# Optimization experiments

Hardware: AMD Instinct MI355X
Metric: run time of the kernel (lower is better)

## Reference

```python
import jax, jax.numpy as jnp
import numpy as np

N_NODES = 50000
N_EDGES = 800000
D = 256


def _mean_aggregate(x, src, tgt, num_nodes):
    # scatter-mean of source features onto target nodes: [N, D]
    summed = jax.ops.segment_sum(x[src], tgt, num_segments=num_nodes)
    count = jax.ops.segment_sum(jnp.ones((src.shape[0],), x.dtype), tgt,
                                num_segments=num_nodes)
    return summed / jnp.maximum(count, 1.0)[:, None]


def _sage_conv(x, src, tgt, W_l, b, W_r):
    # PyG SAGEConv (aggr='mean'): lin_l(mean_j x_j) + lin_r(x_i)
    agg = _mean_aggregate(x, src, tgt, x.shape[0])
    return agg @ W_l + b + x @ W_r


def setup_inputs() -> dict:
    key = jax.random.key(0)
    ks = jax.random.split(key, 8)
    s = 1.0 / np.sqrt(D)
    x = jax.random.normal(ks[0], (N_NODES, D), dtype=jnp.float32)
    edge_index = jax.random.randint(ks[1], (2, N_EDGES), 0, N_NODES, dtype=jnp.int64)
    return {
        "x": x,
        "edge_index": edge_index,
        "W1_l": jax.random.normal(ks[2], (D, D), dtype=jnp.float32) * s,
        "b1": jnp.zeros((D,), dtype=jnp.float32),
        "W1_r": jax.random.normal(ks[3], (D, D), dtype=jnp.float32) * s,
        "W2_l": jax.random.normal(ks[4], (D, D), dtype=jnp.float32) * s,
        "b2": jnp.zeros((D,), dtype=jnp.float32),
        "W2_r": jax.random.normal(ks[5], (D, D), dtype=jnp.float32) * s,
    }


def reference(x, edge_index, W1_l, b1, W1_r, W2_l, b2, W2_r):
    src, tgt = edge_index[0], edge_index[1]
    h = jax.nn.relu(_sage_conv(x, src, tgt, W1_l, b1, W1_r))
    return _sage_conv(h, src, tgt, W2_l, b2, W2_r)
```

## Files before the change

### kernel.cpp

```cpp
#include <hip/hip_runtime.h>
#include <hip/hip_bf16.h>

#define NN 50000
#define NE 800000
#define DD 256
#define KK 512
#define PAD 64
#define CSTR 16

#define FB 3125
#define CB 12500
#define WB 1024

typedef unsigned short u16;
typedef unsigned int   u32;
typedef unsigned char  u8;
typedef __attribute__((ext_vector_type(8))) __bf16 bf16x8;
typedef __attribute__((ext_vector_type(4))) float  f32x4;
typedef __attribute__((ext_vector_type(2))) float  f32x2;
typedef __attribute__((ext_vector_type(8))) u16    u16x8;
typedef __attribute__((ext_vector_type(4))) u16    u16x4;

#define GLOAD_LDS16(g, l) \
  __builtin_amdgcn_global_load_lds((const __attribute__((address_space(1))) void*)(g), \
                                   (__attribute__((address_space(3))) void*)(l), 16, 0, 0)

static __device__ __forceinline__ u16 f2bf(float f) {
  u32 u = __float_as_uint(f);
  u32 r = (u + 0x7FFFu + ((u >> 16) & 1u)) >> 16;
  return (u16)r;
}

__global__ void k_prep(const int* __restrict__ src, const int* __restrict__ tgt,
                       int* __restrict__ cnt, int* __restrict__ col,
                       const float* __restrict__ x, u16* __restrict__ x_bf,
                       u32* __restrict__ x_f8,
                       const float* __restrict__ W1l, const float* __restrict__ W1r,
                       const float* __restrict__ W2l, const float* __restrict__ W2r,
                       u16* __restrict__ Wc1T, u16* __restrict__ Wc2T) {
  const int b = blockIdx.x;
  if (b < FB) {
    int i = b * 256 + threadIdx.x;
    int t = tgt[i];
    int p = atomicAdd(&cnt[t * CSTR], 1);
    if (p < PAD) col[t * PAD + p] = src[i];
  } else if (b < FB + CB) {
    int i = (b - FB) * 256 + threadIdx.x;
    const float4 v = *reinterpret_cast<const float4*>(x + i * 4);
    u16x4 o; o.x = f2bf(v.x); o.y = f2bf(v.y); o.z = f2bf(v.z); o.w = f2bf(v.w);
    *reinterpret_cast<u16x4*>(x_bf + i * 4) = o;
    int pk = __builtin_amdgcn_cvt_pk_fp8_f32(v.x, v.y, 0, false);
    pk = __builtin_amdgcn_cvt_pk_fp8_f32(v.z, v.w, pk, true);
    x_f8[i] = (u32)pk;
  } else {
    int gid = (b - FB - CB) * 256 + threadIdx.x;
    int layer = gid >> 17;
    int idx = gid & 131071;
    int n = idx >> 9, k = idx & 511;
    const float* Wl = layer ? W2l : W1l;
    const float* Wr = layer ? W2r : W1r;
    u16* WcT = layer ? Wc2T : Wc1T;
    float v = (k < DD) ? Wl[k * DD + n] : Wr[(k - DD) * DD + n];
    int reg = k >> 6, ko = k & 63;
    int k2 = (reg << 6) + ((((ko >> 3) ^ (n & 7)) << 3)) + (ko & 7);
    WcT[n * KK + k2] = f2bf(v);
  }
}

__global__ void k_aggregate(const u8* __restrict__ feat8, const int* __restrict__ cnt,
                            const int* __restrict__ col, u16* __restrict__ out) {
  const int wave = threadIdx.x >> 6;
  const int lane = threadIdx.x & 63;
  const int half = lane >> 5;
  const int l32 = lane & 31;
  const int node = blockIdx.x * 4 + wave;
  int deg = cnt[node * CSTR];
  if (deg > PAD) deg = PAD;
  const int s = node * PAD, e = s + deg;
  const int fo = l32 * 8;
  float a[8] = {0.f, 0.f, 0.f, 0.f, 0.f, 0.f, 0.f, 0.f};

#define ACC8(vv)                                                       \
  {                                                                    \
    f32x2 p0 = __builtin_amdgcn_cvt_pk_f32_fp8((int)(vv).x, false);    \
    f32x2 p1 = __builtin_amdgcn_cvt_pk_f32_fp8((int)(vv).x, true);     \
    f32x2 p2 = __builtin_amdgcn_cvt_pk_f32_fp8((int)(vv).y, false);    \
    f32x2 p3 = __builtin_amdgcn_cvt_pk_f32_fp8((int)(vv).y, true);     \
    a[0] += p0.x; a[1] += p0.y; a[2] += p1.x; a[3] += p1.y;            \
    a[4] += p2.x; a[5] += p2.y; a[6] += p3.x; a[7] += p3.y;            \
  }

  int i = s + half;
  for (; i + 6 < e; i += 8) {
    int c0 = col[i], c1 = col[i + 2], c2 = col[i + 4], c3 = col[i + 6];
    uint2 v0 = *reinterpret_cast<const uint2*>(feat8 + c0 * DD + fo);
    uint2 v1 = *reinterpret_cast<const uint2*>(feat8 + c1 * DD + fo);
    uint2 v2 = *reinterpret_cast<const uint2*>(feat8 + c2 * DD + fo);
    uint2 v3 = *reinterpret_cast<const uint2*>(feat8 + c3 * DD + fo);
    ACC8(v0) ACC8(v1) ACC8(v2) ACC8(v3)
  }
  for (; i < e; i += 2) {
    uint2 v = *reinterpret_cast<const uint2*>(feat8 + col[i] * DD + fo);
    ACC8(v)
  }
#undef ACC8
#pragma unroll
  for (int j = 0; j < 8; ++j) a[j] += __shfl_xor(a[j], 32, 64);

  if (half == 0) {
    const float scale = (deg > 0) ? 1.0f / (float)deg : 0.0f;
    u16x8 o;
#pragma unroll
    for (int j = 0; j < 8; ++j) o[j] = f2bf(a[j] * scale);
    *reinterpret_cast<u16x8*>(out + node * DD + fo) = o;
  }
}

#define BM 64
#define BN 256
#define BK 64

template <int LAYER>
__global__ void k_gemm_fused(const u16* __restrict__ A0, const u16* __restrict__ A1,
                             const u16* __restrict__ WcT, const float* __restrict__ bias,
                             u16* __restrict__ outb, u8* __restrict__ outf8,
                             float* __restrict__ outf, int M) {
  __shared__ alignas(16) u16 lA[BM * BK];
  __shared__ alignas(16) u16 lB[BN * BK];
  const int tid = threadIdx.x;
  const int rowBase = blockIdx.x * BM;
  const int wave = tid >> 6, lane = tid & 63;
  const int wc = wave;
  const int l8 = lane >> 3;
  const int ch = lane & 7;

  f32x4 acc[4][4] = {};

  for (int k0 = 0; k0 < KK; k0 += BK) {
    if (k0) __syncthreads();
    const u16* Asrc = (k0 < DD) ? A0 : A1;
    const int kk = k0 & (DD - 1);
#pragma unroll
    for (int j = 0; j < 2; ++j) {
      int row = wave * 16 + j * 8 + l8;
      const u16* g = Asrc + (size_t)(rowBase + row) * DD + kk + ((ch ^ (row & 7)) << 3);
      GLOAD_LDS16(g, &lA[(wave * 16 + j * 8) * BK]);
    }
#pragma unroll
    for (int j = 0; j < 8; ++j) {
      int row = wave * 64 + j * 8 + l8;
      const u16* g = WcT + (size_t)row * KK + k0 + (ch << 3);
      GLOAD_LDS16(g, &lB[(wave * 64 + j * 8) * BK]);
    }
    __syncthreads();

#pragma unroll
    for (int ks = 0; ks < 2; ++ks) {
      const int kbyte = ks * 64 + (lane >> 4) * 16;
      bf16x8 af[4], bfg[4];
#pragma unroll
      for (int m = 0; m < 4; ++m) {
        int row = m * 16 + (lane & 15);
        af[m] = *reinterpret_cast<const bf16x8*>((const char*)lA + row * 128 + (kbyte ^ ((row & 7) << 4)));
      }
#pragma unroll
      for (int n = 0; n < 4; ++n) {
        int row = wc * 64 + n * 16 + (lane & 15);
        bfg[n] = *reinterpret_cast<const bf16x8*>((const char*)lB + row * 128 + (kbyte ^ ((row & 7) << 4)));
      }
#pragma unroll
      for (int m = 0; m < 4; ++m)
#pragma unroll
        for (int n = 0; n < 4; ++n)
          acc[m][n] = __builtin_amdgcn_mfma_f32_16x16x32_bf16(af[m], bfg[n], acc[m][n], 0, 0, 0);
    }
  }

  const int lrow = (lane >> 4) * 4;
  const int lcol = lane & 15;
#pragma unroll
  for (int n = 0; n < 4; ++n) {
    const int gcol = wc * 64 + n * 16 + lcol;
    const float bv = bias[gcol];
#pragma unroll
    for (int m = 0; m < 4; ++m) {
#pragma unroll
      for (int r = 0; r < 4; ++r) {
        const int grow = rowBase + m * 16 + lrow + r;
        if (grow < M) {
          float v = acc[m][n][r] + bv;
          if (LAYER == 1) {
            v = fmaxf(v, 0.0f);
            outb[grow * DD + gcol] = f2bf(v);
            int pk = __builtin_amdgcn_cvt_pk_fp8_f32(v, 0.0f, 0, false);
            outf8[grow * DD + gcol] = (u8)(pk & 0xff);
          } else {
            outf[grow * DD + gcol] = v;
          }
        }
      }
    }
  }
}

extern "C" void kernel_launch(void* const* d_in, const int* in_sizes, int n_in,
                              void* d_out, int out_size, void* d_ws, size_t ws_size,
                              hipStream_t stream) {
  const float* x    = (const float*)d_in[0];
  const int*   ei   = (const int*)d_in[1];
  const float* W1l  = (const float*)d_in[2];
  const float* b1   = (const float*)d_in[3];
  const float* W1r  = (const float*)d_in[4];
  const float* W2l  = (const float*)d_in[5];
  const float* b2   = (const float*)d_in[6];
  const float* W2r  = (const float*)d_in[7];
  float* out = (float*)d_out;

  const int* srcIdx = ei;
  const int* tgtIdx = ei + NE;

  char* ws = (char*)d_ws;
  int* cnt    = (int*)(ws + 0);
  int* col    = (int*)(ws + 3200000);
  u16* x_bf   = (u16*)(ws + 16000000);
  u16* h_bf   = (u16*)(ws + 41600000);
  u16* agg_bf = (u16*)(ws + 67200000);
  u8*  x_f8   = (u8*) (ws + 92800000);
  u8*  h_f8   = (u8*) (ws + 105600000);
  u16* Wc1T   = (u16*)(ws + 118400000);
  u16* Wc2T   = (u16*)(ws + 118662144);

  hipMemsetAsync(cnt, 0, NN * CSTR * sizeof(int), stream);
  k_prep<<<FB + CB + WB, 256, 0, stream>>>(srcIdx, tgtIdx, cnt, col, x, x_bf,
                                           (u32*)x_f8,
                                           W1l, W1r, W2l, W2r, Wc1T, Wc2T);

  const int ggrid = (NN + BM - 1) / BM;

  k_aggregate<<<NN / 4, 256, 0, stream>>>(x_f8, cnt, col, agg_bf);
  k_gemm_fused<1><<<ggrid, 256, 0, stream>>>(agg_bf, x_bf, Wc1T, b1, h_bf, h_f8, nullptr, NN);
  k_aggregate<<<NN / 4, 256, 0, stream>>>(h_f8, cnt, col, agg_bf);
  k_gemm_fused<2><<<ggrid, 256, 0, stream>>>(agg_bf, h_bf, Wc2T, b2, nullptr, nullptr, out, NN);
}
```

Baseline: 200.5 us.

## Double GEMM row tile and interleave edge-bucketing with feature conversion blocks

The fused GEMM row tile grows from 64 to 128 rows, so each B-weight tile loaded into LDS is reused across twice as many rows. A-fragments are now loaded per m-step rather than all held at once, and out-of-range rows are clamped for loads. Separately, the prep kernel interleaves the atomic edge-bucketing blocks with the x conversion blocks, so atomic-heavy and bandwidth-heavy work run at the same time. The cost is double the accumulator registers, which may lower occupancy, and half as many GEMM blocks.

```diff
diff --git a/kernel.cpp b/kernel.cpp
--- a/kernel.cpp
+++ b/kernel.cpp
@@ -11,6 +11,7 @@
 #define FB 3125
 #define CB 12500
 #define WB 1024
+#define PREP_GRID (2 * FB + (CB - FB) + WB)
 
 typedef unsigned short u16;
 typedef unsigned int   u32;
@@ -39,13 +40,25 @@
                        const float* __restrict__ W2l, const float* __restrict__ W2r,
                        u16* __restrict__ Wc1T, u16* __restrict__ Wc2T) {
   const int b = blockIdx.x;
-  if (b < FB) {
-    int i = b * 256 + threadIdx.x;
+  int role, idx;
+  if (b < 2 * FB) {
+    role = b & 1;
+    idx = b >> 1;
+  } else if (b < 2 * FB + (CB - FB)) {
+    role = 1;
+    idx = FB + (b - 2 * FB);
+  } else {
+    role = 2;
+    idx = b - (2 * FB + (CB - FB));
+  }
+
+  if (role == 0) {
+    int i = idx * 256 + threadIdx.x;
     int t = tgt[i];
     int p = atomicAdd(&cnt[t * CSTR], 1);
     if (p < PAD) col[t * PAD + p] = src[i];
-  } else if (b < FB + CB) {
-    int i = (b - FB) * 256 + threadIdx.x;
+  } else if (role == 1) {
+    int i = idx * 256 + threadIdx.x;
     const float4 v = *reinterpret_cast<const float4*>(x + i * 4);
     u16x4 o; o.x = f2bf(v.x); o.y = f2bf(v.y); o.z = f2bf(v.z); o.w = f2bf(v.w);
     *reinterpret_cast<u16x4*>(x_bf + i * 4) = o;
@@ -53,10 +66,10 @@
     pk = __builtin_amdgcn_cvt_pk_fp8_f32(v.z, v.w, pk, true);
     x_f8[i] = (u32)pk;
   } else {
-    int gid = (b - FB - CB) * 256 + threadIdx.x;
+    int gid = idx * 256 + threadIdx.x;
     int layer = gid >> 17;
-    int idx = gid & 131071;
-    int n = idx >> 9, k = idx & 511;
+    int idx2 = gid & 131071;
+    int n = idx2 >> 9, k = idx2 & 511;
     const float* Wl = layer ? W2l : W1l;
     const float* Wr = layer ? W2r : W1r;
     u16* WcT = layer ? Wc2T : Wc1T;
@@ -116,7 +129,7 @@
   }
 }
 
-#define BM 64
+#define BM 128
 #define BN 256
 #define BK 64
 
@@ -134,17 +147,19 @@
   const int l8 = lane >> 3;
   const int ch = lane & 7;
 
-  f32x4 acc[4][4] = {};
+  f32x4 acc[8][4] = {};
 
   for (int k0 = 0; k0 < KK; k0 += BK) {
     if (k0) __syncthreads();
     const u16* Asrc = (k0 < DD) ? A0 : A1;
     const int kk = k0 & (DD - 1);
 #pragma unroll
-    for (int j = 0; j < 2; ++j) {
-      int row = wave * 16 + j * 8 + l8;
-      const u16* g = Asrc + (size_t)(rowBase + row) * DD + kk + ((ch ^ (row & 7)) << 3);
-      GLOAD_LDS16(g, &lA[(wave * 16 + j * 8) * BK]);
+    for (int j = 0; j < 4; ++j) {
+      int row = wave * 32 + j * 8 + l8;
+      int grow = rowBase + row;
+      int gr = (grow < M) ? grow : 0;
+      const u16* g = Asrc + (size_t)gr * DD + kk + ((ch ^ (row & 7)) << 3);
+      GLOAD_LDS16(g, &lA[(wave * 32 + j * 8) * BK]);
     }
 #pragma unroll
     for (int j = 0; j < 8; ++j) {
@@ -157,22 +172,20 @@
 #pragma unroll
     for (int ks = 0; ks < 2; ++ks) {
       const int kbyte = ks * 64 + (lane >> 4) * 16;
-      bf16x8 af[4], bfg[4];
-#pragma unroll
-      for (int m = 0; m < 4; ++m) {
-        int row = m * 16 + (lane & 15);
-        af[m] = *reinterpret_cast<const bf16x8*>((const char*)lA + row * 128 + (kbyte ^ ((row & 7) << 4)));
-      }
+      bf16x8 bfg[4];
 #pragma unroll
       for (int n = 0; n < 4; ++n) {
         int row = wc * 64 + n * 16 + (lane & 15);
         bfg[n] = *reinterpret_cast<const bf16x8*>((const char*)lB + row * 128 + (kbyte ^ ((row & 7) << 4)));
       }
 #pragma unroll
-      for (int m = 0; m < 4; ++m)
+      for (int m = 0; m < 8; ++m) {
+        int row = m * 16 + (lane & 15);
+        bf16x8 af = *reinterpret_cast<const bf16x8*>((const char*)lA + row * 128 + (kbyte ^ ((row & 7) << 4)));
 #pragma unroll
         for (int n = 0; n < 4; ++n)
-          acc[m][n] = __builtin_amdgcn_mfma_f32_16x16x32_bf16(af[m], bfg[n], acc[m][n], 0, 0, 0);
+          acc[m][n] = __builtin_amdgcn_mfma_f32_16x16x32_bf16(af, bfg[n], acc[m][n], 0, 0, 0);
+      }
     }
   }
 
@@ -183,7 +196,7 @@
     const int gcol = wc * 64 + n * 16 + lcol;
     const float bv = bias[gcol];
 #pragma unroll
-    for (int m = 0; m < 4; ++m) {
+    for (int m = 0; m < 8; ++m) {
 #pragma unroll
       for (int r = 0; r < 4; ++r) {
         const int grow = rowBase + m * 16 + lrow + r;
@@ -231,9 +244,9 @@
   u16* Wc2T   = (u16*)(ws + 118662144);
 
   hipMemsetAsync(cnt, 0, NN * CSTR * sizeof(int), stream);
-  k_prep<<<FB + CB + WB, 256, 0, stream>>>(srcIdx, tgtIdx, cnt, col, x, x_bf,
-                                           (u32*)x_f8,
-                                           W1l, W1r, W2l, W2r, Wc1T, Wc2T);
+  k_prep<<<PREP_GRID, 256, 0, stream>>>(srcIdx, tgtIdx, cnt, col, x, x_bf,
+                                        (u32*)x_f8,
+                                        W1l, W1r, W2l, W2r, Wc1T, Wc2T);
 
   const int ggrid = (NN + BM - 1) / BM;
 
```

Measured after the change: 401.2 us. 2x slower.
